# Kernel tuning notes

Hardware: AMD Instinct MI355X
Metric: run time of the kernel (lower is better)

The kernel has to match this reference:

```python
import jax, jax.numpy as jnp
import numpy as np

N, IN_DIM, OUT_DIM, HEADS = 50000, 256, 256, 8
C = OUT_DIM // HEADS  # per-head channels = 32
E = 800000
G = 64  # number of graphs in the batch
NEG_SLOPE = 0.2
GN_EPS = 1e-5


def setup_inputs() -> dict:
    key = jax.random.key(0)
    ks = jax.random.split(key, 12)
    x = jax.random.normal(ks[0], (N, IN_DIM), dtype=jnp.float32)
    edge_index = jax.random.randint(ks[1], (2, E), 0, N, dtype=jnp.int64)
    batch = jnp.sort(jax.random.randint(ks[2], (N,), 0, G, dtype=jnp.int64))
    s = 1.0 / np.sqrt(IN_DIM)
    W_l = jax.random.uniform(ks[3], (IN_DIM, HEADS * C), jnp.float32, -s, s)
    b_l = jnp.zeros((HEADS * C,), jnp.float32)
    W_r = jax.random.uniform(ks[4], (IN_DIM, HEADS * C), jnp.float32, -s, s)
    b_r = jnp.zeros((HEADS * C,), jnp.float32)
    att = jax.random.normal(ks[5], (HEADS, C), dtype=jnp.float32) / np.sqrt(C)
    bias = jnp.zeros((HEADS * C,), jnp.float32)
    gn_weight = jnp.ones((OUT_DIM,), jnp.float32)
    gn_bias = jnp.zeros((OUT_DIM,), jnp.float32)
    gn_mean_scale = jnp.ones((OUT_DIM,), jnp.float32)
    return {"x": x, "edge_index": edge_index, "batch": batch,
            "W_l": W_l, "b_l": b_l, "W_r": W_r, "b_r": b_r,
            "att": att, "bias": bias, "gn_weight": gn_weight,
            "gn_bias": gn_bias, "gn_mean_scale": gn_mean_scale}


def _gat_block(x, src, dst, batch, W_l, b_l, W_r, b_r, att, bias,
               gn_weight, gn_bias, gn_mean_scale):
    n = x.shape[0]
    # GATv2Conv (add_self_loops=True, concat=True)
    loops = jnp.arange(n, dtype=src.dtype)
    src = jnp.concatenate([src, loops])
    dst = jnp.concatenate([dst, loops])
    xl = (x @ W_l + b_l).reshape(n, HEADS, C)  # source transform
    xr = (x @ W_r + b_r).reshape(n, HEADS, C)  # target transform
    e = jax.nn.leaky_relu(xl[src] + xr[dst], NEG_SLOPE)  # [E', H, C]
    logits = jnp.einsum('ehc,hc->eh', e, att)            # [E', H]
    # segment softmax over incoming edges of each destination node
    m = jax.ops.segment_max(logits, dst, num_segments=n)
    alpha = jnp.exp(logits - m[dst])
    denom = jax.ops.segment_sum(alpha, dst, num_segments=n)
    alpha = alpha / (denom[dst] + 1e-16)
    msg = xl[src] * alpha[:, :, None]                    # [E', H, C]
    h = jax.ops.segment_sum(msg, dst, num_segments=n).reshape(n, HEADS * C) + bias
    # identity residual (in_dim == out_dim) + ELU
    h = jax.nn.elu(h + x)
    # GraphNorm (post-norm)
    counts = jnp.maximum(jax.ops.segment_sum(jnp.ones((n,), h.dtype), batch,
                                             num_segments=G), 1.0)
    mean = jax.ops.segment_sum(h, batch, num_segments=G) / counts[:, None]
    out0 = h - gn_mean_scale * mean[batch]
    var = jax.ops.segment_sum(out0 * out0, batch, num_segments=G) / counts[:, None]
    return gn_weight * out0 / jnp.sqrt(var[batch] + GN_EPS) + gn_bias


def reference(x, edge_index, batch, W_l, b_l, W_r, b_r, att, bias,
              gn_weight, gn_bias, gn_mean_scale):
    return _gat_block(x, edge_index[0], edge_index[1], batch,
                      W_l, b_l, W_r, b_r, att, bias,
                      gn_weight, gn_bias, gn_mean_scale)
```

## Files before the change

kernel.cpp:

```cpp
#include <hip/hip_runtime.h>
#include <hip/hip_bf16.h>
#include <stdint.h>

#define N_NODES 50000
#define MPAD    50048
#define IN_DIM  256
#define EDGES   800000
#define EPRIME  (EDGES + N_NODES)
#define NGRAPH  64
#define GN_EPS  1e-5f
#define ECPAD   53248
#define SEG     52
#define SEG4    13

typedef __attribute__((ext_vector_type(8))) short short8;
typedef __attribute__((ext_vector_type(4))) float floatx4;

__device__ __forceinline__ unsigned short f2b(float f) {
    uint32_t u = __float_as_uint(f);
    u += 0x7fffu + ((u >> 16) & 1u);
    return (unsigned short)(u >> 16);
}
__device__ __forceinline__ float b2f(unsigned short u) {
    return __uint_as_float(((uint32_t)u) << 16);
}

__global__ __launch_bounds__(256) void k_prep_w(const float* __restrict__ Wl,
                                                const float* __restrict__ Wr,
                                                unsigned short* __restrict__ Wt) {
    int idx = blockIdx.x * 256 + threadIdx.x;
    int n = idx >> 8, k = idx & 255;
    float v = (n < 256) ? Wl[k * 256 + n] : Wr[k * 256 + (n - 256)];
    Wt[idx] = f2b(v);
}

__global__ __launch_bounds__(512) void k_gemm(const float* __restrict__ x,
                                              const unsigned short* __restrict__ Wt,
                                              const float* __restrict__ bl,
                                              const float* __restrict__ br,
                                              unsigned short* __restrict__ XL,
                                              unsigned short* __restrict__ XR) {
    __shared__ unsigned short As[64 * 256];
    int rbase = blockIdx.x * 64;
    int tid = threadIdx.x;

#pragma unroll
    for (int it = 0; it < 4; ++it) {
        int c = it * 512 + tid;
        int row = c >> 5, ch = c & 31;
        int gr = rbase + row;
        float4 f0, f1;
        if (gr < N_NODES) {
            const float4* src = (const float4*)(x + (size_t)gr * 256 + ch * 8);
            f0 = src[0]; f1 = src[1];
        } else {
            f0 = make_float4(0.f,0.f,0.f,0.f); f1 = f0;
        }
        short8 hv;
        hv[0] = (short)f2b(f0.x); hv[1] = (short)f2b(f0.y);
        hv[2] = (short)f2b(f0.z); hv[3] = (short)f2b(f0.w);
        hv[4] = (short)f2b(f1.x); hv[5] = (short)f2b(f1.y);
        hv[6] = (short)f2b(f1.z); hv[7] = (short)f2b(f1.w);
        *(short8*)(As + row * 256 + (ch ^ (row & 7)) * 8) = hv;
    }
    __syncthreads();

    int w = tid >> 6;
    int l = tid & 63;
    int m = l & 15, q = l >> 4;

    floatx4 acc[4][4];
#pragma unroll
    for (int rf = 0; rf < 4; ++rf)
#pragma unroll
        for (int cf = 0; cf < 4; ++cf)
            acc[rf][cf] = (floatx4){0.f, 0.f, 0.f, 0.f};

    const unsigned short* wbase = Wt + (size_t)(w * 64) * 256;

#pragma unroll
    for (int kk = 0; kk < 8; ++kk) {
        short8 a[4];
#pragma unroll
        for (int rf = 0; rf < 4; ++rf) {
            int row = rf * 16 + m;
            int ch = (kk * 4 + q) ^ (row & 7);
            a[rf] = *(const short8*)(As + row * 256 + ch * 8);
        }
#pragma unroll
        for (int cf = 0; cf < 4; ++cf) {
            short8 b = *(const short8*)(wbase + (size_t)(cf * 16 + m) * 256 + kk * 32 + q * 8);
#pragma unroll
            for (int rf = 0; rf < 4; ++rf)
                acc[rf][cf] = __builtin_amdgcn_mfma_f32_16x16x32_bf16(b, a[rf], acc[rf][cf], 0, 0, 0);
        }
    }

    unsigned short* obase = (w < 4) ? XL : XR;
    const float* bptr = (w < 4) ? bl : br;
    int cb = (w & 3) * 64;
#pragma unroll
    for (int cf = 0; cf < 4; ++cf) {
        int chb = cb + cf * 16 + q * 4;
        float4 bv = *(const float4*)(bptr + chb);
#pragma unroll
        for (int rf = 0; rf < 4; ++rf) {
            int node = rbase + rf * 16 + m;
            ushort4 o;
            o.x = f2b(acc[rf][cf][0] + bv.x);
            o.y = f2b(acc[rf][cf][1] + bv.y);
            o.z = f2b(acc[rf][cf][2] + bv.z);
            o.w = f2b(acc[rf][cf][3] + bv.w);
            *(ushort4*)(obase + (size_t)node * 256 + chb) = o;
        }
    }
}

__global__ __launch_bounds__(256) void k_hist(const int* __restrict__ ei,
                                              const int* __restrict__ batch,
                                              int* __restrict__ ecount,
                                              int* __restrict__ ncount) {
    __shared__ int hist[NGRAPH];
    if (threadIdx.x < NGRAPH) hist[threadIdx.x] = 0;
    __syncthreads();
    int e = blockIdx.x * 256 + threadIdx.x;
    if (e < EPRIME) {
        int d = (e < EDGES) ? ei[EDGES + e] : (e - EDGES);
        atomicAdd(&ecount[d], 1);
    }
    if (e < N_NODES) atomicAdd(&hist[batch[e]], 1);
    __syncthreads();
    if (threadIdx.x < NGRAPH && hist[threadIdx.x])
        atomicAdd(&ncount[threadIdx.x], hist[threadIdx.x]);
}

__global__ __launch_bounds__(1024) void k_scan(const int* __restrict__ ecount,
                                               int* __restrict__ estart,
                                               int* __restrict__ ecursor) {
    __shared__ int buf[1024];
    int t = threadIdx.x;
    int base = t * SEG;
    int4 v[SEG4];
    int sum = 0;
#pragma unroll
    for (int j = 0; j < SEG4; ++j) {
        v[j] = ((const int4*)(ecount + base))[j];
        sum += v[j].x + v[j].y + v[j].z + v[j].w;
    }
    buf[t] = sum;
    __syncthreads();
    for (int off = 1; off < 1024; off <<= 1) {
        int p = (t >= off) ? buf[t - off] : 0;
        __syncthreads();
        buf[t] += p;
        __syncthreads();
    }
    int run = buf[t] - sum;
#pragma unroll
    for (int j = 0; j < SEG4; ++j) {
        int4 o;
        o.x = run; run += v[j].x;
        o.y = run; run += v[j].y;
        o.z = run; run += v[j].z;
        o.w = run; run += v[j].w;
        ((int4*)(estart + base))[j]  = o;
        ((int4*)(ecursor + base))[j] = o;
    }
}

__global__ __launch_bounds__(256) void k_scatter(const int* __restrict__ ei,
                                                 int* __restrict__ ecursor,
                                                 int* __restrict__ sedge) {
    int e = blockIdx.x * 256 + threadIdx.x;
    if (e >= EPRIME) return;
    int s, d;
    if (e < EDGES) { s = ei[e]; d = ei[EDGES + e]; }
    else           { s = d = e - EDGES; }
    int pos = atomicAdd(&ecursor[d], 1);
    sedge[pos] = s;
}

__global__ __launch_bounds__(256) void k_msg(const unsigned short* __restrict__ XL,
                                             const unsigned short* __restrict__ XRb,
                                             const float* __restrict__ x,
                                             const float* __restrict__ att,
                                             const float* __restrict__ bias,
                                             const int* __restrict__ sedge,
                                             const int* __restrict__ estart,
                                             const int* __restrict__ ecount,
                                             float* __restrict__ out) {
    int d = (int)((blockIdx.x * 256 + threadIdx.x) >> 6);
    int l = threadIdx.x & 63;

    ushort4 xrb = ((const ushort4*)(XRb + (size_t)d * 256))[l];
    float xr0 = b2f(xrb.x), xr1 = b2f(xrb.y), xr2 = b2f(xrb.z), xr3 = b2f(xrb.w);
    float4 attv = ((const float4*)att)[l];
    int s0  = estart[d];
    int cnt = ecount[d];

    float den0 = 0.f, den1 = 0.f;
    float a0 = 0.f, a1 = 0.f, a2 = 0.f, a3 = 0.f;
    float b0 = 0.f, b1 = 0.f, b2 = 0.f, b3 = 0.f;

    auto ldrow = [&](int src) -> ushort4 {
        return ((const ushort4*)(XL + (size_t)src * 256))[l];
    };

#define PROC(XB, DEN, C0, C1, C2, C3)                                   \
    {                                                                   \
        float x0 = b2f(XB.x), x1 = b2f(XB.y), x2 = b2f(XB.z), x3 = b2f(XB.w); \
        float e0 = x0 + xr0; e0 = fmaxf(e0, 0.2f * e0);                 \
        float e1 = x1 + xr1; e1 = fmaxf(e1, 0.2f * e1);                 \
        float e2 = x2 + xr2; e2 = fmaxf(e2, 0.2f * e2);                 \
        float e3 = x3 + xr3; e3 = fmaxf(e3, 0.2f * e3);                 \
        float pp = (e0 * attv.x + e1 * attv.y) + (e2 * attv.z + e3 * attv.w); \
        pp += __shfl_xor(pp, 1);                                        \
        pp += __shfl_xor(pp, 2);                                        \
        pp += __shfl_xor(pp, 4);                                        \
        float al = __expf(fminf(pp, 80.f));                             \
        DEN += al;                                                      \
        C0 = fmaf(al, x0, C0); C1 = fmaf(al, x1, C1);                   \
        C2 = fmaf(al, x2, C2); C3 = fmaf(al, x3, C3);                   \
    }

    int npair = cnt >> 1, rem = cnt & 1;
    ushort4 A0 = ldrow(sedge[s0]);
    ushort4 A1 = ldrow(sedge[s0 + (cnt > 1 ? 1 : 0)]);

    for (int p = 0; p < npair; ++p) {
        ushort4 B0 = A0, B1 = A1;
        int nb = s0 + 2 * p + 2;
        if (p + 1 < npair) {
            int sa = sedge[nb], sb = sedge[nb + 1];
            A0 = ldrow(sa);
            A1 = ldrow(sb);
        } else if (rem) {
            A0 = ldrow(sedge[s0 + cnt - 1]);
        }
        PROC(B0, den0, a0, a1, a2, a3);
        PROC(B1, den1, b0, b1, b2, b3);
    }
    if (rem) PROC(A0, den0, a0, a1, a2, a3);
#undef PROC

    float inv = 1.f / (den0 + den1 + 1e-16f);
    a0 += b0; a1 += b1; a2 += b2; a3 += b3;

    float4 xin = ((const float4*)(x + (size_t)d * 256))[l];
    float4 bv  = ((const float4*)bias)[l];
    float h0 = a0 * inv + bv.x + xin.x; h0 = (h0 > 0.f) ? h0 : (__expf(h0) - 1.f);
    float h1 = a1 * inv + bv.y + xin.y; h1 = (h1 > 0.f) ? h1 : (__expf(h1) - 1.f);
    float h2 = a2 * inv + bv.z + xin.z; h2 = (h2 > 0.f) ? h2 : (__expf(h2) - 1.f);
    float h3 = a3 * inv + bv.w + xin.w; h3 = (h3 > 0.f) ? h3 : (__expf(h3) - 1.f);
    ((float4*)(out + (size_t)d * 256))[l] = make_float4(h0, h1, h2, h3);
}

#define GN_ROWS 128
__global__ __launch_bounds__(256) void k_gn_sum(const float* __restrict__ h,
                                                const int* __restrict__ batch,
                                                float* __restrict__ gsum,
                                                float* __restrict__ gsq) {
    __shared__ int bsh[GN_ROWS];
    int r0 = blockIdx.x * GN_ROWS;
    for (int j = threadIdx.x; j < GN_ROWS; j += 256) {
        int i = r0 + j;
        bsh[j] = (i < N_NODES) ? batch[i] : -1;
    }
    __syncthreads();
    int c = threadIdx.x;
    float s1 = 0.f, s2 = 0.f;
    int g = bsh[0];
    for (int j = 0; j < GN_ROWS; ++j) {
        int i = r0 + j;
        if (i >= N_NODES) break;
        int bg = bsh[j];
        if (bg != g) {
            atomicAdd(&gsum[g * 256 + c], s1);
            atomicAdd(&gsq[g * 256 + c], s2);
            s1 = 0.f; s2 = 0.f; g = bg;
        }
        float v = h[(size_t)i * 256 + c];
        s1 += v; s2 += v * v;
    }
    atomicAdd(&gsum[g * 256 + c], s1);
    atomicAdd(&gsq[g * 256 + c], s2);
}

__global__ __launch_bounds__(256) void k_final(float* __restrict__ out,
                                               const int* __restrict__ batch,
                                               const float* __restrict__ gsum,
                                               const float* __restrict__ gsq,
                                               const int* __restrict__ ncount,
                                               const float* __restrict__ gnw,
                                               const float* __restrict__ gnb,
                                               const float* __restrict__ gms) {
    int idx = blockIdx.x * 256 + threadIdx.x;
    int i = idx >> 6, l = idx & 63;
    if (i >= N_NODES) return;
    int g = batch[i];
    float inv = 1.f / fmaxf((float)ncount[g], 1.f);
    float4 hv = ((const float4*)(out + (size_t)i * 256))[l];
    float4 ms = ((const float4*)(gsum + g * 256))[l];
    float4 qs = ((const float4*)(gsq  + g * 256))[l];
    float4 wv = ((const float4*)gnw)[l];
    float4 bv = ((const float4*)gnb)[l];
    float4 sv = ((const float4*)gms)[l];
    float4 o;
    {
        float m = ms.x * inv, q = qs.x * inv;
        o.x = wv.x * (hv.x - sv.x * m) * rsqrtf(q - m * m * sv.x * (2.f - sv.x) + GN_EPS) + bv.x;
    }
    {
        float m = ms.y * inv, q = qs.y * inv;
        o.y = wv.y * (hv.y - sv.y * m) * rsqrtf(q - m * m * sv.y * (2.f - sv.y) + GN_EPS) + bv.y;
    }
    {
        float m = ms.z * inv, q = qs.z * inv;
        o.z = wv.z * (hv.z - sv.z * m) * rsqrtf(q - m * m * sv.z * (2.f - sv.z) + GN_EPS) + bv.z;
    }
    {
        float m = ms.w * inv, q = qs.w * inv;
        o.w = wv.w * (hv.w - sv.w * m) * rsqrtf(q - m * m * sv.w * (2.f - sv.w) + GN_EPS) + bv.w;
    }
    ((float4*)(out + (size_t)i * 256))[l] = o;
}

extern "C" void kernel_launch(void* const* d_in, const int* in_sizes, int n_in,
                              void* d_out, int out_size, void* d_ws, size_t ws_size,
                              hipStream_t stream) {
    const float* x    = (const float*)d_in[0];
    const int*   ei   = (const int*)d_in[1];
    const int*   batch= (const int*)d_in[2];
    const float* Wl   = (const float*)d_in[3];
    const float* bl   = (const float*)d_in[4];
    const float* Wr   = (const float*)d_in[5];
    const float* br   = (const float*)d_in[6];
    const float* att  = (const float*)d_in[7];
    const float* bias = (const float*)d_in[8];
    const float* gnw  = (const float*)d_in[9];
    const float* gnb  = (const float*)d_in[10];
    const float* gms  = (const float*)d_in[11];
    float* out = (float*)d_out;

    char* p = (char*)d_ws;
    auto alloc = [&](size_t bytes) -> char* {
        char* r = p;
        p += (bytes + 255) & ~(size_t)255;
        return r;
    };
    unsigned short* Wt  = (unsigned short*)alloc((size_t)512 * 256 * 2);
    unsigned short* XL  = (unsigned short*)alloc((size_t)MPAD * 256 * 2);
    unsigned short* XRb = (unsigned short*)alloc((size_t)MPAD * 256 * 2);
    int* ecount         = (int*)alloc((size_t)ECPAD * 4);
    int* estart         = (int*)alloc((size_t)ECPAD * 4);
    int* ecursor        = (int*)alloc((size_t)ECPAD * 4);
    int* sedge          = (int*)alloc((size_t)EPRIME * 4);
    int* ncount         = (int*)alloc((size_t)NGRAPH * 4);
    float* gsum         = (float*)alloc((size_t)2 * NGRAPH * 256 * 4);
    float* gsq          = gsum + NGRAPH * 256;

    hipMemsetAsync(ecount, 0, (size_t)ECPAD * 4, stream);
    hipMemsetAsync(ncount, 0, (size_t)NGRAPH * 4, stream);
    hipMemsetAsync(gsum,   0, (size_t)2 * NGRAPH * 256 * 4, stream);

    k_prep_w<<<512, 256, 0, stream>>>(Wl, Wr, Wt);
    k_gemm<<<MPAD / 64, 512, 0, stream>>>(x, Wt, bl, br, XL, XRb);

    k_hist<<<(EPRIME + 255) / 256, 256, 0, stream>>>(ei, batch, ecount, ncount);
    k_scan<<<1, 1024, 0, stream>>>(ecount, estart, ecursor);
    k_scatter<<<(EPRIME + 255) / 256, 256, 0, stream>>>(ei, ecursor, sedge);

    k_msg<<<N_NODES / 4, 256, 0, stream>>>(XL, XRb, x, att, bias,
                                           sedge, estart, ecount, out);

    k_gn_sum<<<(N_NODES + GN_ROWS - 1) / GN_ROWS, 256, 0, stream>>>(out, batch, gsum, gsq);
    k_final<<<N_NODES * 64 / 256, 256, 0, stream>>>(out, batch, gsum, gsq,
                                                    ncount, gnw, gnb, gms);
}
```

Before: 409.6 us.

## Deepen edge gather prefetch to four rows and merge workspace memsets

```diff
diff --git a/kernel.cpp b/kernel.cpp
--- a/kernel.cpp
+++ b/kernel.cpp
@@ -15,6 +15,7 @@
 
 typedef __attribute__((ext_vector_type(8))) short short8;
 typedef __attribute__((ext_vector_type(4))) float floatx4;
+typedef __attribute__((ext_vector_type(2))) float float2v;
 
 __device__ __forceinline__ unsigned short f2b(float f) {
     uint32_t u = __float_as_uint(f);
@@ -191,67 +192,94 @@
                                              float* __restrict__ out) {
     int d = (int)((blockIdx.x * 256 + threadIdx.x) >> 6);
     int l = threadIdx.x & 63;
-
-    ushort4 xrb = ((const ushort4*)(XRb + (size_t)d * 256))[l];
-    float xr0 = b2f(xrb.x), xr1 = b2f(xrb.y), xr2 = b2f(xrb.z), xr3 = b2f(xrb.w);
+    int lofs = l * 8;
+
+    float4 xin  = ((const float4*)(x + (size_t)d * 256))[l];
+    float4 bvv  = ((const float4*)bias)[l];
     float4 attv = ((const float4*)att)[l];
-    int s0  = estart[d];
-    int cnt = ecount[d];
-
-    float den0 = 0.f, den1 = 0.f;
-    float a0 = 0.f, a1 = 0.f, a2 = 0.f, a3 = 0.f;
-    float b0 = 0.f, b1 = 0.f, b2 = 0.f, b3 = 0.f;
-
-    auto ldrow = [&](int src) -> ushort4 {
-        return ((const ushort4*)(XL + (size_t)src * 256))[l];
+    float2v att01 = {attv.x, attv.y}, att23 = {attv.z, attv.w};
+
+    uint2 xru = ((const uint2*)(XRb + (size_t)d * 256))[l];
+    float2v xr01, xr23;
+    xr01[0] = __uint_as_float(xru.x << 16);
+    xr01[1] = __uint_as_float(xru.x & 0xffff0000u);
+    xr23[0] = __uint_as_float(xru.y << 16);
+    xr23[1] = __uint_as_float(xru.y & 0xffff0000u);
+
+    int s0  = __builtin_amdgcn_readfirstlane(estart[d]);
+    int cnt = __builtin_amdgcn_readfirstlane(ecount[d]);
+    int c1m = cnt - 1;
+
+    auto ldrow = [&](int src) -> uint2 {
+        size_t off = ((size_t)(uint32_t)__builtin_amdgcn_readfirstlane(src)) << 9;
+        return *(const uint2*)((const char*)XL + off + lofs);
     };
 
-#define PROC(XB, DEN, C0, C1, C2, C3)                                   \
-    {                                                                   \
-        float x0 = b2f(XB.x), x1 = b2f(XB.y), x2 = b2f(XB.z), x3 = b2f(XB.w); \
-        float e0 = x0 + xr0; e0 = fmaxf(e0, 0.2f * e0);                 \
-        float e1 = x1 + xr1; e1 = fmaxf(e1, 0.2f * e1);                 \
-        float e2 = x2 + xr2; e2 = fmaxf(e2, 0.2f * e2);                 \
-        float e3 = x3 + xr3; e3 = fmaxf(e3, 0.2f * e3);                 \
-        float pp = (e0 * attv.x + e1 * attv.y) + (e2 * attv.z + e3 * attv.w); \
-        pp += __shfl_xor(pp, 1);                                        \
-        pp += __shfl_xor(pp, 2);                                        \
-        pp += __shfl_xor(pp, 4);                                        \
-        float al = __expf(fminf(pp, 80.f));                             \
-        DEN += al;                                                      \
-        C0 = fmaf(al, x0, C0); C1 = fmaf(al, x1, C1);                   \
-        C2 = fmaf(al, x2, C2); C3 = fmaf(al, x3, C3);                   \
-    }
-
-    int npair = cnt >> 1, rem = cnt & 1;
-    ushort4 A0 = ldrow(sedge[s0]);
-    ushort4 A1 = ldrow(sedge[s0 + (cnt > 1 ? 1 : 0)]);
-
-    for (int p = 0; p < npair; ++p) {
-        ushort4 B0 = A0, B1 = A1;
-        int nb = s0 + 2 * p + 2;
-        if (p + 1 < npair) {
-            int sa = sedge[nb], sb = sedge[nb + 1];
-            A0 = ldrow(sa);
-            A1 = ldrow(sb);
-        } else if (rem) {
-            A0 = ldrow(sedge[s0 + cnt - 1]);
-        }
-        PROC(B0, den0, a0, a1, a2, a3);
-        PROC(B1, den1, b0, b1, b2, b3);
-    }
-    if (rem) PROC(A0, den0, a0, a1, a2, a3);
-#undef PROC
-
-    float inv = 1.f / (den0 + den1 + 1e-16f);
-    a0 += b0; a1 += b1; a2 += b2; a3 += b3;
-
-    float4 xin = ((const float4*)(x + (size_t)d * 256))[l];
-    float4 bv  = ((const float4*)bias)[l];
-    float h0 = a0 * inv + bv.x + xin.x; h0 = (h0 > 0.f) ? h0 : (__expf(h0) - 1.f);
-    float h1 = a1 * inv + bv.y + xin.y; h1 = (h1 > 0.f) ? h1 : (__expf(h1) - 1.f);
-    float h2 = a2 * inv + bv.z + xin.z; h2 = (h2 > 0.f) ? h2 : (__expf(h2) - 1.f);
-    float h3 = a3 * inv + bv.w + xin.w; h3 = (h3 > 0.f) ? h3 : (__expf(h3) - 1.f);
+    float den0 = 0.f, den1 = 0.f, den2 = 0.f, den3 = 0.f;
+    float2v A01 = {0.f,0.f}, A23 = {0.f,0.f};
+    float2v B01 = {0.f,0.f}, B23 = {0.f,0.f};
+    float2v C01 = {0.f,0.f}, C23 = {0.f,0.f};
+    float2v D01 = {0.f,0.f}, D23 = {0.f,0.f};
+
+    auto proc = [&](uint2 U, float& den, float2v& R01, float2v& R23) {
+        float2v x01, x23;
+        x01[0] = __uint_as_float(U.x << 16);
+        x01[1] = __uint_as_float(U.x & 0xffff0000u);
+        x23[0] = __uint_as_float(U.y << 16);
+        x23[1] = __uint_as_float(U.y & 0xffff0000u);
+        float2v e01 = x01 + xr01, e23 = x23 + xr23;
+        float2v f01 = e01 * 0.2f, f23 = e23 * 0.2f;
+        e01[0] = fmaxf(e01[0], f01[0]); e01[1] = fmaxf(e01[1], f01[1]);
+        e23[0] = fmaxf(e23[0], f23[0]); e23[1] = fmaxf(e23[1], f23[1]);
+        float2v pp2 = e01 * att01 + e23 * att23;
+        float pp = pp2[0] + pp2[1];
+        {
+            int pi = __float_as_int(pp);
+            pp += __int_as_float(__builtin_amdgcn_update_dpp(0, pi, 0xB1, 0xF, 0xF, true));
+            pi = __float_as_int(pp);
+            pp += __int_as_float(__builtin_amdgcn_update_dpp(0, pi, 0x4E, 0xF, 0xF, true));
+            pp += __shfl_xor(pp, 4);
+        }
+        float al = __expf(fminf(pp, 80.f));
+        den += al;
+        float2v al2 = {al, al};
+        R01 += al2 * x01;
+        R23 += al2 * x23;
+    };
+
+    uint2 P0 = ldrow(sedge[s0]);
+    uint2 P1 = ldrow(sedge[s0 + min(1, c1m)]);
+    uint2 P2 = ldrow(sedge[s0 + min(2, c1m)]);
+    uint2 P3 = ldrow(sedge[s0 + min(3, c1m)]);
+
+    int nq = cnt >> 2;
+    for (int qq = 0; qq < nq; ++qq) {
+        uint2 Q0 = P0, Q1 = P1, Q2 = P2, Q3 = P3;
+        int nb = (qq + 1) << 2;
+        int i0 = min(nb,     c1m), i1 = min(nb + 1, c1m);
+        int i2 = min(nb + 2, c1m), i3 = min(nb + 3, c1m);
+        P0 = ldrow(sedge[s0 + i0]);
+        P1 = ldrow(sedge[s0 + i1]);
+        P2 = ldrow(sedge[s0 + i2]);
+        P3 = ldrow(sedge[s0 + i3]);
+        proc(Q0, den0, A01, A23);
+        proc(Q1, den1, B01, B23);
+        proc(Q2, den2, C01, C23);
+        proc(Q3, den3, D01, D23);
+    }
+    int rem = cnt & 3;
+    if (rem > 0) proc(P0, den0, A01, A23);
+    if (rem > 1) proc(P1, den1, B01, B23);
+    if (rem > 2) proc(P2, den2, C01, C23);
+
+    float inv = 1.f / ((den0 + den1) + (den2 + den3) + 1e-16f);
+    A01 = (A01 + B01) + (C01 + D01);
+    A23 = (A23 + B23) + (C23 + D23);
+
+    float h0 = A01[0] * inv + bvv.x + xin.x; h0 = (h0 > 0.f) ? h0 : (__expf(h0) - 1.f);
+    float h1 = A01[1] * inv + bvv.y + xin.y; h1 = (h1 > 0.f) ? h1 : (__expf(h1) - 1.f);
+    float h2 = A23[0] * inv + bvv.z + xin.z; h2 = (h2 > 0.f) ? h2 : (__expf(h2) - 1.f);
+    float h3 = A23[1] * inv + bvv.w + xin.w; h3 = (h3 > 0.f) ? h3 : (__expf(h3) - 1.f);
     ((float4*)(out + (size_t)d * 256))[l] = make_float4(h0, h1, h2, h3);
 }
 
@@ -351,17 +379,15 @@
     unsigned short* Wt  = (unsigned short*)alloc((size_t)512 * 256 * 2);
     unsigned short* XL  = (unsigned short*)alloc((size_t)MPAD * 256 * 2);
     unsigned short* XRb = (unsigned short*)alloc((size_t)MPAD * 256 * 2);
-    int* ecount         = (int*)alloc((size_t)ECPAD * 4);
     int* estart         = (int*)alloc((size_t)ECPAD * 4);
     int* ecursor        = (int*)alloc((size_t)ECPAD * 4);
     int* sedge          = (int*)alloc((size_t)EPRIME * 4);
+    int* ecount         = (int*)alloc((size_t)ECPAD * 4);
     int* ncount         = (int*)alloc((size_t)NGRAPH * 4);
     float* gsum         = (float*)alloc((size_t)2 * NGRAPH * 256 * 4);
     float* gsq          = gsum + NGRAPH * 256;
-
-    hipMemsetAsync(ecount, 0, (size_t)ECPAD * 4, stream);
-    hipMemsetAsync(ncount, 0, (size_t)NGRAPH * 4, stream);
-    hipMemsetAsync(gsum,   0, (size_t)2 * NGRAPH * 256 * 4, stream);
+    size_t zbytes = (size_t)((char*)(gsum + 2 * NGRAPH * 256) - (char*)ecount);
+    hipMemsetAsync(ecount, 0, zbytes, stream);
 
     k_prep_w<<<512, 256, 0, stream>>>(Wl, Wr, Wt);
     k_gemm<<<MPAD / 64, 512, 0, stream>>>(x, Wt, bl, br, XL, XRb);
```

Result: no change. 404.9 us (-1.1%).
